# Kernel tuning notes

Measured on AMD Instinct MI355X. Metric: run time of the kernel, lower is better.

## Reference

```python
import jax, jax.numpy as jnp
import numpy as np

B, D_IN, H, C = 8192, 2048, 1024, 1000
LAYERS = [0, 1, 2, 3, 4]          # structure.layers
N_MAIN = 4                        # main hidden layers for layers[1:]
# skip layers in __init__ enumeration order: (target_layer, source_layer)
SKIPS = [(2, 0), (3, 0), (3, 1), (4, 0), (4, 1), (4, 2)]


def _linear_init(key, out_f, in_f):
    k1, k2 = jax.random.split(key)
    bound = 1.0 / np.sqrt(in_f)
    W = jax.random.uniform(k1, (out_f, in_f), minval=-bound, maxval=bound, dtype=jnp.float32)
    b = jax.random.uniform(k2, (out_f,), minval=-bound, maxval=bound, dtype=jnp.float32)
    return W, b


def setup_inputs() -> dict:
    key = jax.random.key(0)
    ks = iter(jax.random.split(key, 40))
    x = jax.random.normal(next(ks), (B, D_IN), dtype=jnp.float32)

    Wf, bf = _linear_init(next(ks), H, D_IN)
    mf = jax.random.bernoulli(next(ks), 0.5, (H, D_IN))

    main_W, main_b, main_m = [], [], []
    for _ in range(N_MAIN):
        W, b = _linear_init(next(ks), H, H)
        main_W.append(W); main_b.append(b)
        main_m.append(jax.random.bernoulli(next(ks), 0.5, (H, H)))

    skip_W, skip_b, skip_m = [], [], []
    for _ in SKIPS:
        W, b = _linear_init(next(ks), H, H)
        skip_W.append(W); skip_b.append(b)
        skip_m.append(jax.random.bernoulli(next(ks), 0.5, (H, H)))

    Wo, bo = _linear_init(next(ks), C, H)
    mo = jax.random.bernoulli(next(ks), 0.5, (C, H))

    return {"x": x, "Wf": Wf, "bf": bf, "mf": mf,
            "main_W": main_W, "main_b": main_b, "main_m": main_m,
            "skip_W": skip_W, "skip_b": skip_b, "skip_m": skip_m,
            "Wo": Wo, "bo": bo, "mo": mo}


def _masked_linear(x, W, b, m):
    # F.linear(x, weight * mask, bias): mask applied to weight before GEMM
    return x @ (W * m).T + b


def reference(x, Wf, bf, mf, main_W, main_b, main_m, skip_W, skip_b, skip_m, Wo, bo, mo):
    relu = jax.nn.relu
    last = relu(_masked_linear(x, Wf, bf, mf))        # layer 0 output, [B, H]
    results = {0: last}
    for i, layer_idx in enumerate(LAYERS[1:]):
        out = relu(_masked_linear(last, main_W[i], main_b[i], main_m[i]))
        for k, (tgt, src) in enumerate(SKIPS):
            if tgt == layer_idx:
                out = out + relu(_masked_linear(results[src], skip_W[k], skip_b[k], skip_m[k]))
        results[layer_idx] = out
        last = out
    return _masked_linear(last, Wo, bo, mo)            # [B, C]
```

## Files before the change

### kernel.cpp

```cpp
#include <hip/hip_runtime.h>
#include <hip/hip_bf16.h>
#include <stdint.h>


typedef unsigned short ushort_t;
typedef __bf16 bf16x8 __attribute__((ext_vector_type(8)));
typedef float f32x4 __attribute__((ext_vector_type(4)));

__device__ __forceinline__ void gl_lds16(const void* g, void* l) {
  typedef __attribute__((address_space(1))) void gvoid;
  typedef __attribute__((address_space(3))) void lvoid;
  __builtin_amdgcn_global_load_lds((gvoid*)(void*)g, (lvoid*)l, 16, 0, 0);
}

__device__ __forceinline__ ushort_t f2b(float f) {
  __hip_bfloat16 h = (__hip_bfloat16)f;
  return *(ushort_t*)&h;
}

__global__ void detect_kernel(const ushort_t* x, const ushort_t* mf, int* flags) {
  __shared__ int s[4];
  if (threadIdx.x < 4) s[threadIdx.x] = 0;
  __syncthreads();
  int expout = 0, m3f80_even = 0, m3f80_odd = 0, mhi01 = 0;
  for (int k = threadIdx.x; k < 2048; k += 256) {
    ushort_t w = x[k];
    int e = (w >> 7) & 0xFF;
    if (e < 96 || e > 144) expout++;
    ushort_t mw = mf[k];
    if (mw == 0x3F80) { if (k & 1) m3f80_odd++; else m3f80_even++; }
    if ((mw >> 8) == 1) mhi01++;
  }
  atomicAdd(&s[0], expout);
  atomicAdd(&s[1], m3f80_even);
  atomicAdd(&s[2], m3f80_odd);
  atomicAdd(&s[3], mhi01);
  __syncthreads();
  if (threadIdx.x == 0) {
    flags[0] = (s[0] > 100) ? 1 : 0;
    int mmode = 0;
    if (s[1] > 100) mmode = 2;
    else if (s[2] > 100) mmode = 3;
    else if (s[3] > 200) mmode = 1;
    flags[1] = mmode;
  }
}

struct PrepEnt {
  const void* w; size_t woff;
  const void* m; size_t moff;
  ushort_t* o;
  int n;
  int valid;
};
struct PrepAll { PrepEnt e[25]; };

__global__ void prep_weights(PrepAll p, const int* flags) {
  const bool f32 = flags[0] != 0;
  const int mmode = flags[1];
  const PrepEnt e = p.e[blockIdx.y];
  const int nch = e.n >> 3;
  const int stride = blockDim.x * gridDim.x;
  for (int ci = blockIdx.x * blockDim.x + threadIdx.x; ci < nch; ci += stride) {
    const int i = ci << 3;
    ushort_t o[8] = {0, 0, 0, 0, 0, 0, 0, 0};
    if (i < e.valid) {
      ushort_t wb[8];
      if (f32) {
        const float* wp = (const float*)e.w + e.woff + i;
        float4 a = *(const float4*)wp;
        float4 b = *(const float4*)(wp + 4);
        wb[0] = f2b(a.x); wb[1] = f2b(a.y); wb[2] = f2b(a.z); wb[3] = f2b(a.w);
        wb[4] = f2b(b.x); wb[5] = f2b(b.y); wb[6] = f2b(b.z); wb[7] = f2b(b.w);
      } else {
        *(uint4*)wb = *(const uint4*)((const ushort_t*)e.w + e.woff + i);
      }
      unsigned mk = 0xFF;
      if (e.m) {
        mk = 0;
        if (mmode == 0) {
          const int4* mp = (const int4*)((const int*)e.m + e.moff + i);
          int4 a = mp[0], b = mp[1];
          mk = (a.x != 0) | ((a.y != 0) << 1) | ((a.z != 0) << 2) | ((a.w != 0) << 3) |
               ((b.x != 0) << 4) | ((b.y != 0) << 5) | ((b.z != 0) << 6) | ((b.w != 0) << 7);
        } else if (mmode == 1) {
          const uint2 mv = *(const uint2*)((const unsigned char*)e.m + e.moff + i);
          const unsigned char* mb = (const unsigned char*)&mv;
          for (int j = 0; j < 8; j++) mk |= (mb[j] != 0) << j;
        } else if (mmode == 2) {
          uint4 mv = *(const uint4*)((const ushort_t*)e.m + e.moff + i);
          const ushort_t* ms = (const ushort_t*)&mv;
          for (int j = 0; j < 8; j++) mk |= (ms[j] != 0) << j;
        } else {
          const uint4* mp = (const uint4*)((const unsigned int*)e.m + e.moff + i);
          uint4 a = mp[0], b = mp[1];
          const unsigned* u = (const unsigned*)&a;
          const unsigned* v = (const unsigned*)&b;
          for (int j = 0; j < 4; j++) mk |= (u[j] != 0) << j;
          for (int j = 0; j < 4; j++) mk |= (v[j] != 0) << (4 + j);
        }
      }
#pragma unroll
      for (int j = 0; j < 8; j++) o[j] = ((mk >> j) & 1) ? wb[j] : (ushort_t)0;
    }
    *(uint4*)(e.o + i) = *(uint4*)o;
  }
}

struct GemmSrc { const ushort_t* A; const ushort_t* B; const ushort_t* bias; };
struct GemmArgs { GemmSrc s[4]; };

template <int NSRC, bool RELU, bool NGUARD>
__launch_bounds__(256, 2)
__global__ void gemm_multi(GemmArgs args, void* Cv, const int* of32flag,
                           int K, int N_real, int ldc)
{
  __shared__ __align__(16) ushort_t As[2][128 * 32];
  __shared__ __align__(16) ushort_t Bs[2][128 * 32];

  const bool of32 = (of32flag != nullptr) && (of32flag[0] != 0);
  __hip_bfloat16* C = (__hip_bfloat16*)Cv;
  float* Cf = (float*)Cv;

  const int tid  = threadIdx.x;
  const int lane = tid & 63;
  const int wave = tid >> 6;
  const int wm = (wave >> 1) * 64;
  const int wn = (wave & 1) * 64;
  const int fr = lane & 15;
  const int kg = lane >> 4;

  const int lid = blockIdx.y * 8 + blockIdx.x;
  const int s8  = lid >> 3;
  const int bm  = ((lid & 7) * 8 + (s8 >> 3)) * 128;
  const int bn  = (s8 & 7) * 128;

  const int srow = tid >> 2;
  const int scol = (((tid & 3) ^ ((srow >> 1) & 3)) * 8);
  const size_t aoff = (size_t)(bm + srow) * K + scol;
  const size_t boff = (size_t)(bn + srow) * K + scol;
  const size_t rowskip = (size_t)64 * K;

  auto stage = [&](const ushort_t* gA, const ushort_t* gB, int buf) {
    ushort_t* lA = &As[buf][wave * 512];
    ushort_t* lB = &Bs[buf][wave * 512];
    gl_lds16(gA, lA);
    gl_lds16(gA + rowskip, lA + 2048);
    gl_lds16(gB, lB);
    gl_lds16(gB + rowskip, lB + 2048);
  };

  f32x4 acc[4][4], out_acc[4][4];
#pragma unroll
  for (int i = 0; i < 4; i++)
#pragma unroll
    for (int j = 0; j < 4; j++) {
      acc[i][j] = (f32x4){0.f, 0.f, 0.f, 0.f};
      out_acc[i][j] = (f32x4){0.f, 0.f, 0.f, 0.f};
    }

  stage(args.s[0].A + aoff, args.s[0].B + boff, 0);
  int cur = 0;

  const int sw = kg ^ ((fr >> 1) & 3);

#pragma unroll
  for (int s = 0; s < NSRC; ++s) {
    const ushort_t* gA = args.s[s].A + aoff;
    const ushort_t* gB = args.s[s].B + boff;
    for (int k0 = 0; k0 < K; k0 += 32) {
      __syncthreads();
      if (k0 + 32 < K) {
        stage(gA + k0 + 32, gB + k0 + 32, cur ^ 1);
      } else if (s + 1 < NSRC) {
        stage(args.s[s + 1].A + aoff, args.s[s + 1].B + boff, cur ^ 1);
      }

      const bf16x8* Asv = (const bf16x8*)As[cur];
      const bf16x8* Bsv = (const bf16x8*)Bs[cur];
      bf16x8 af[4], bfr[4];
#pragma unroll
      for (int i = 0; i < 4; i++) af[i]  = Asv[(wm + i * 16 + fr) * 4 + sw];
#pragma unroll
      for (int i = 0; i < 4; i++) bfr[i] = Bsv[(wn + i * 16 + fr) * 4 + sw];
#pragma unroll
      for (int mi = 0; mi < 4; mi++)
#pragma unroll
        for (int ni = 0; ni < 4; ni++)
          acc[mi][ni] = __builtin_amdgcn_mfma_f32_16x16x32_bf16(
              af[mi], bfr[ni], acc[mi][ni], 0, 0, 0);
      cur ^= 1;
    }

    if (NSRC > 1) {
      const ushort_t* bias = args.s[s].bias;
#pragma unroll
      for (int ni = 0; ni < 4; ni++) {
        const int c = bn + wn + ni * 16 + fr;
        const float bb = (float)*(const __hip_bfloat16*)(bias + c);
#pragma unroll
        for (int mi = 0; mi < 4; mi++)
#pragma unroll
          for (int j = 0; j < 4; j++) {
            float v = acc[mi][ni][j] + bb;
            if (RELU) v = fmaxf(v, 0.0f);
            out_acc[mi][ni][j] += v;
            acc[mi][ni][j] = 0.0f;
          }
      }
    }
  }

#pragma unroll
  for (int ni = 0; ni < 4; ni++) {
    const int c = bn + wn + ni * 16 + fr;
    if (NGUARD && c >= N_real) continue;
    float bb = 0.0f;
    if (NSRC == 1) bb = (float)*(const __hip_bfloat16*)(args.s[0].bias + c);
#pragma unroll
    for (int mi = 0; mi < 4; mi++) {
      const int r0 = bm + wm + mi * 16 + kg * 4;
#pragma unroll
      for (int j = 0; j < 4; j++) {
        const size_t idx = (size_t)(r0 + j) * ldc + c;
        float v;
        if (NSRC == 1) {
          v = acc[mi][ni][j] + bb;
          if (RELU) v = fmaxf(v, 0.0f);
        } else {
          v = out_acc[mi][ni][j];
        }
        if (of32) Cf[idx] = v;
        else      C[idx]  = (__hip_bfloat16)v;
      }
    }
  }
}

extern "C" void kernel_launch(void* const* d_in, const int* in_sizes, int n_in,
                              void* d_out, int out_size, void* d_ws, size_t ws_size,
                              hipStream_t stream) {
  (void)out_size; (void)ws_size;
  const int Bm = 8192, DIN = 2048, H = 1024, Cn = 1000;
  const size_t HH = (size_t)H * H;

  struct PO { const void* p; size_t off; };
  PO x{d_in[0], 0}, Wf{d_in[0], 0}, mf{d_in[0], 0}, Wo{d_in[0], 0}, mo{d_in[0], 0};
  PO bf{d_in[0], 0}, bo{d_in[0], 0};
  PO mW[4], mM[4], mB[4], sW[6], sM[6], sB[6];
  for (int i = 0; i < 4; i++) { mW[i] = {d_in[0], 0}; mM[i] = mW[i]; mB[i] = mW[i]; }
  for (int i = 0; i < 6; i++) { sW[i] = {d_in[0], 0}; sM[i] = sW[i]; sB[i] = sW[i]; }

  {
    int c2M = 0, c1M = 0, c1k = 0, cWoMo = 0, c4 = 0, c6 = 0;
    for (int i = 0; i < n_in; i++) {
      const int s = in_sizes[i];
      const void* p = d_in[i];
      switch (s) {
        case 16777216: x = {p, 0}; break;
        case 2097152:  if (c2M++ == 0) Wf = {p, 0}; else mf = {p, 0}; break;
        case 1048576: {
          int j = c1M++;
          if (j < 4)       mW[j]      = {p, 0};
          else if (j < 8)  mM[j - 4]  = {p, 0};
          else if (j < 14) sW[j - 8]  = {p, 0};
          else if (j < 20) sM[j - 14] = {p, 0};
          break;
        }
        case 1024: {
          int j = c1k++;
          if (j == 0)      bf        = {p, 0};
          else if (j < 5)  mB[j - 1] = {p, 0};
          else if (j < 11) sB[j - 5] = {p, 0};
          break;
        }
        case 1024000: if (cWoMo++ == 0) Wo = {p, 0}; else mo = {p, 0}; break;
        case 1000: bo = {p, 0}; break;
        case 4194304:
          for (int t = 0; t < 4; t++) {
            if (c4 == 0) mW[t] = {p, t * HH}; else mM[t] = {p, t * HH};
          }
          c4++; break;
        case 6291456:
          for (int t = 0; t < 6; t++) {
            if (c6 == 0) sW[t] = {p, t * HH}; else sM[t] = {p, t * HH};
          }
          c6++; break;
        case 4096:
          for (int t = 0; t < 4; t++) mB[t] = {p, (size_t)t * H};
          break;
        case 6144:
          for (int t = 0; t < 6; t++) sB[t] = {p, (size_t)t * H};
          break;
        default: break;
      }
    }
  }

  ushort_t* wsp = (ushort_t*)d_ws;
  size_t off = 0;
  int* flags = (int*)wsp; off += 32;
  ushort_t* xc = wsp + off; off += (size_t)Bm * DIN;
  __hip_bfloat16* r[5];
  for (int i = 0; i < 5; i++) { r[i] = (__hip_bfloat16*)(wsp + off); off += (size_t)Bm * H; }
  ushort_t* wWf = wsp + off; off += (size_t)H * DIN;
  ushort_t* wMain[4];
  for (int i = 0; i < 4; i++) { wMain[i] = wsp + off; off += HH; }
  ushort_t* wSkip[6];
  for (int k = 0; k < 6; k++) { wSkip[k] = wsp + off; off += HH; }
  ushort_t* wWo = wsp + off; off += (size_t)1024 * 1024;
  ushort_t* cbf_ = wsp + off; off += 1024;
  ushort_t* cmB[4];
  for (int i = 0; i < 4; i++) { cmB[i] = wsp + off; off += 1024; }
  ushort_t* csB[6];
  for (int k = 0; k < 6; k++) { csB[k] = wsp + off; off += 1024; }
  ushort_t* cbo = wsp + off; off += 1024;

  detect_kernel<<<1, 256, 0, stream>>>((const ushort_t*)x.p, (const ushort_t*)mf.p, flags);

  PrepAll p;
  p.e[0]  = { Wf.p, Wf.off, mf.p, mf.off, wWf, H * DIN, H * DIN };
  for (int i = 0; i < 4; i++)
    p.e[1 + i] = { mW[i].p, mW[i].off, mM[i].p, mM[i].off, wMain[i], (int)HH, (int)HH };
  for (int k = 0; k < 6; k++)
    p.e[5 + k] = { sW[k].p, sW[k].off, sM[k].p, sM[k].off, wSkip[k], (int)HH, (int)HH };
  p.e[11] = { Wo.p, Wo.off, mo.p, mo.off, wWo, 1024 * 1024, Cn * H };
  p.e[12] = { bf.p, bf.off, nullptr, 0, cbf_, H, H };
  for (int i = 0; i < 4; i++)
    p.e[13 + i] = { mB[i].p, mB[i].off, nullptr, 0, cmB[i], H, H };
  for (int k = 0; k < 6; k++)
    p.e[17 + k] = { sB[k].p, sB[k].off, nullptr, 0, csB[k], H, H };
  p.e[23] = { bo.p, bo.off, nullptr, 0, cbo, 1024, Cn };
  p.e[24] = { x.p, x.off, nullptr, 0, xc, Bm * DIN, Bm * DIN };
  prep_weights<<<dim3(256, 25), dim3(256), 0, stream>>>(p, flags);

  const dim3 g(8, 64), b(256);

  GemmArgs a0; a0.s[0] = { xc, wWf, cbf_ };
  gemm_multi<1, true, false><<<g, b, 0, stream>>>(a0, r[0], nullptr, DIN, H, H);

  GemmArgs a1; a1.s[0] = { (ushort_t*)r[0], wMain[0], cmB[0] };
  gemm_multi<1, true, false><<<g, b, 0, stream>>>(a1, r[1], nullptr, H, H, H);

  GemmArgs a2;
  a2.s[0] = { (ushort_t*)r[1], wMain[1], cmB[1] };
  a2.s[1] = { (ushort_t*)r[0], wSkip[0], csB[0] };
  gemm_multi<2, true, false><<<g, b, 0, stream>>>(a2, r[2], nullptr, H, H, H);

  GemmArgs a3;
  a3.s[0] = { (ushort_t*)r[2], wMain[2], cmB[2] };
  a3.s[1] = { (ushort_t*)r[0], wSkip[1], csB[1] };
  a3.s[2] = { (ushort_t*)r[1], wSkip[2], csB[2] };
  gemm_multi<3, true, false><<<g, b, 0, stream>>>(a3, r[3], nullptr, H, H, H);

  GemmArgs a4;
  a4.s[0] = { (ushort_t*)r[3], wMain[3], cmB[3] };
  a4.s[1] = { (ushort_t*)r[0], wSkip[3], csB[3] };
  a4.s[2] = { (ushort_t*)r[1], wSkip[4], csB[4] };
  a4.s[3] = { (ushort_t*)r[2], wSkip[5], csB[5] };
  gemm_multi<4, true, false><<<g, b, 0, stream>>>(a4, r[4], nullptr, H, H, H);

  GemmArgs ao; ao.s[0] = { (ushort_t*)r[4], wWo, cbo };
  gemm_multi<1, false, true><<<g, b, 0, stream>>>(ao, d_out, flags, H, Cn, Cn);
}
```

Before: 558.6 us.

## Restructure GEMM to 256x128 tiles, 8 waves, BK=64 with phased MFMA/LDS schedule

Each block now computes a 256x128 output tile with 512 threads (8 waves), stages 64-wide K slices into a double-buffered LDS with an XOR swizzle, and splits each K-step into four quadrant phases. LDS fragment loads are interleaved with MFMA bursts under explicit s_barrier, waitcnt and s_setprio control. Bias values are preloaded once per block. The goal is more reuse per loaded tile, fewer barriers per FLOP and better overlap of global-to-LDS prefetch with matrix math, at the cost of larger LDS use, higher register pressure and hand-tuned synchronization that must stay correct.

Result: faster. 535.4 us (-4.2%).

```diff
diff --git a/kernel.cpp b/kernel.cpp
--- a/kernel.cpp
+++ b/kernel.cpp
@@ -110,13 +110,17 @@
 struct GemmSrc { const ushort_t* A; const ushort_t* B; const ushort_t* bias; };
 struct GemmArgs { GemmSrc s[4]; };
 
+#define SBAR()  asm volatile("s_barrier" ::: "memory")
+#define LGKM0() asm volatile("s_waitcnt lgkmcnt(0)" ::: "memory")
+#define VMC6()  asm volatile("s_waitcnt vmcnt(6)" ::: "memory")
+#define VMC0()  asm volatile("s_waitcnt vmcnt(0)" ::: "memory")
+
 template <int NSRC, bool RELU, bool NGUARD>
-__launch_bounds__(256, 2)
+__launch_bounds__(512, 2)
 __global__ void gemm_multi(GemmArgs args, void* Cv, const int* of32flag,
                            int K, int N_real, int ldc)
 {
-  __shared__ __align__(16) ushort_t As[2][128 * 32];
-  __shared__ __align__(16) ushort_t Bs[2][128 * 32];
+  __shared__ __align__(16) ushort_t lds[2][24576];
 
   const bool of32 = (of32flag != nullptr) && (of32flag[0] != 0);
   __hip_bfloat16* C = (__hip_bfloat16*)Cv;
@@ -130,25 +134,32 @@
   const int fr = lane & 15;
   const int kg = lane >> 4;
 
-  const int lid = blockIdx.y * 8 + blockIdx.x;
-  const int s8  = lid >> 3;
-  const int bm  = ((lid & 7) * 8 + (s8 >> 3)) * 128;
-  const int bn  = (s8 & 7) * 128;
-
-  const int srow = tid >> 2;
-  const int scol = (((tid & 3) ^ ((srow >> 1) & 3)) * 8);
-  const size_t aoff = (size_t)(bm + srow) * K + scol;
-  const size_t boff = (size_t)(bn + srow) * K + scol;
-  const size_t rowskip = (size_t)64 * K;
+  const int lid = blockIdx.x;
+  const int xcd = lid & 7, chunk = lid >> 3;
+  const int bm = (xcd * 4 + (chunk >> 3)) * 256;
+  const int bn = (chunk & 7) * 128;
+
+  const int rbase = tid >> 3;
+  const int sg    = (tid & 7) ^ (rbase & 7);
+  const size_t aoff = (size_t)(bm + rbase) * K + sg * 8;
+  const size_t boff = (size_t)(bn + rbase) * K + sg * 8;
+  const size_t rs64 = (size_t)64 * K;
 
   auto stage = [&](const ushort_t* gA, const ushort_t* gB, int buf) {
-    ushort_t* lA = &As[buf][wave * 512];
-    ushort_t* lB = &Bs[buf][wave * 512];
-    gl_lds16(gA, lA);
-    gl_lds16(gA + rowskip, lA + 2048);
-    gl_lds16(gB, lB);
-    gl_lds16(gB + rowskip, lB + 2048);
+    ushort_t* base = &lds[buf][0];
+    ushort_t* lA = base + wave * 512;
+    ushort_t* lB = base + 16384 + wave * 512;
+    gl_lds16(gA,            lA);
+    gl_lds16(gA + rs64,     lA + 4096);
+    gl_lds16(gA + 2 * rs64, lA + 8192);
+    gl_lds16(gA + 3 * rs64, lA + 12288);
+    gl_lds16(gB,            lB);
+    gl_lds16(gB + rs64,     lB + 4096);
   };
+
+  const int s0   = (kg ^ (fr & 7)) * 16;
+  const int arow = (wm + fr) * 128;
+  const int brow = 32768 + (wn + fr) * 128;
 
   f32x4 acc[4][4], out_acc[4][4];
 #pragma unroll
@@ -156,67 +167,149 @@
 #pragma unroll
     for (int j = 0; j < 4; j++) {
       acc[i][j] = (f32x4){0.f, 0.f, 0.f, 0.f};
-      out_acc[i][j] = (f32x4){0.f, 0.f, 0.f, 0.f};
-    }
+      if (NSRC > 1) out_acc[i][j] = (f32x4){0.f, 0.f, 0.f, 0.f};
+    }
+
+  float bpre[NSRC][4];
+#pragma unroll
+  for (int s = 0; s < NSRC; ++s)
+#pragma unroll
+    for (int ni = 0; ni < 4; ni++)
+      bpre[s][ni] = (float)*(const __hip_bfloat16*)
+          (args.s[s].bias + bn + wn + ni * 16 + fr);
+
+  const int TPS = K >> 6;
+  const int NT  = TPS * NSRC;
 
   stage(args.s[0].A + aoff, args.s[0].B + boff, 0);
+  {
+    const int s1 = 1 / TPS, k1 = (1 % TPS) * 64;
+    stage(args.s[s1].A + aoff + k1, args.s[s1].B + boff + k1, 1);
+  }
+  VMC6();
+  SBAR();
+
+  int psrc = 2 / TPS, pk0 = (2 % TPS) * 64;
+  int csrc = 0, ck = 0;
   int cur = 0;
 
-  const int sw = kg ^ ((fr >> 1) & 3);
-
-#pragma unroll
-  for (int s = 0; s < NSRC; ++s) {
-    const ushort_t* gA = args.s[s].A + aoff;
-    const ushort_t* gB = args.s[s].B + boff;
-    for (int k0 = 0; k0 < K; k0 += 32) {
-      __syncthreads();
-      if (k0 + 32 < K) {
-        stage(gA + k0 + 32, gB + k0 + 32, cur ^ 1);
-      } else if (s + 1 < NSRC) {
-        stage(args.s[s + 1].A + aoff, args.s[s + 1].B + boff, cur ^ 1);
-      }
-
-      const bf16x8* Asv = (const bf16x8*)As[cur];
-      const bf16x8* Bsv = (const bf16x8*)Bs[cur];
-      bf16x8 af[4], bfr[4];
-#pragma unroll
-      for (int i = 0; i < 4; i++) af[i]  = Asv[(wm + i * 16 + fr) * 4 + sw];
-#pragma unroll
-      for (int i = 0; i < 4; i++) bfr[i] = Bsv[(wn + i * 16 + fr) * 4 + sw];
-#pragma unroll
-      for (int mi = 0; mi < 4; mi++)
-#pragma unroll
-        for (int ni = 0; ni < 4; ni++)
-          acc[mi][ni] = __builtin_amdgcn_mfma_f32_16x16x32_bf16(
-              af[mi], bfr[ni], acc[mi][ni], 0, 0, 0);
-      cur ^= 1;
-    }
-
-    if (NSRC > 1) {
-      const ushort_t* bias = args.s[s].bias;
-#pragma unroll
-      for (int ni = 0; ni < 4; ni++) {
-        const int c = bn + wn + ni * 16 + fr;
-        const float bb = (float)*(const __hip_bfloat16*)(bias + c);
+  for (int t = 0; t < NT; ++t) {
+    const char* Lb = (const char*)&lds[cur][0];
+    bf16x8 aL[2][2], aH[2][2], bL[2][2], bH[2][2];
+
+#pragma unroll
+    for (int m = 0; m < 2; ++m)
+#pragma unroll
+      for (int ks = 0; ks < 2; ++ks)
+        aL[m][ks] = *(const bf16x8*)(Lb + arow + m * 2048 + (s0 ^ (ks * 64)));
+#pragma unroll
+    for (int n = 0; n < 2; ++n)
+#pragma unroll
+      for (int ks = 0; ks < 2; ++ks)
+        bL[n][ks] = *(const bf16x8*)(Lb + brow + n * 2048 + (s0 ^ (ks * 64)));
+    SBAR();
+    LGKM0();
+    __builtin_amdgcn_s_setprio(1);
+#pragma unroll
+    for (int m = 0; m < 2; ++m)
+#pragma unroll
+      for (int n = 0; n < 2; ++n)
+#pragma unroll
+        for (int ks = 0; ks < 2; ++ks)
+          acc[m][n] = __builtin_amdgcn_mfma_f32_16x16x32_bf16(
+              aL[m][ks], bL[n][ks], acc[m][n], 0, 0, 0);
+    __builtin_amdgcn_s_setprio(0);
+    SBAR();
+
+#pragma unroll
+    for (int n = 0; n < 2; ++n)
+#pragma unroll
+      for (int ks = 0; ks < 2; ++ks)
+        bH[n][ks] = *(const bf16x8*)(Lb + brow + (n + 2) * 2048 + (s0 ^ (ks * 64)));
+    SBAR();
+    LGKM0();
+    __builtin_amdgcn_s_setprio(1);
+#pragma unroll
+    for (int m = 0; m < 2; ++m)
+#pragma unroll
+      for (int n = 0; n < 2; ++n)
+#pragma unroll
+        for (int ks = 0; ks < 2; ++ks)
+          acc[m][n + 2] = __builtin_amdgcn_mfma_f32_16x16x32_bf16(
+              aL[m][ks], bH[n][ks], acc[m][n + 2], 0, 0, 0);
+    __builtin_amdgcn_s_setprio(0);
+    SBAR();
+
+#pragma unroll
+    for (int m = 0; m < 2; ++m)
+#pragma unroll
+      for (int ks = 0; ks < 2; ++ks)
+        aH[m][ks] = *(const bf16x8*)(Lb + arow + (m + 2) * 2048 + (s0 ^ (ks * 64)));
+    SBAR();
+    LGKM0();
+    __builtin_amdgcn_s_setprio(1);
+#pragma unroll
+    for (int m = 0; m < 2; ++m)
+#pragma unroll
+      for (int n = 0; n < 2; ++n)
+#pragma unroll
+        for (int ks = 0; ks < 2; ++ks)
+          acc[m + 2][n] = __builtin_amdgcn_mfma_f32_16x16x32_bf16(
+              aH[m][ks], bL[n][ks], acc[m + 2][n], 0, 0, 0);
+    __builtin_amdgcn_s_setprio(0);
+    SBAR();
+
+    ck += 64;
+    const bool srcEnd = (ck == K);
+    const bool more2 = (t + 2 < NT);
+    if (more2) {
+      stage(args.s[psrc].A + aoff + pk0, args.s[psrc].B + boff + pk0, cur);
+      pk0 += 64; if (pk0 == K) { pk0 = 0; ++psrc; }
+    }
+    __builtin_amdgcn_s_setprio(1);
+#pragma unroll
+    for (int m = 0; m < 2; ++m)
+#pragma unroll
+      for (int n = 0; n < 2; ++n)
+#pragma unroll
+        for (int ks = 0; ks < 2; ++ks)
+          acc[m + 2][n + 2] = __builtin_amdgcn_mfma_f32_16x16x32_bf16(
+              aH[m][ks], bH[n][ks], acc[m + 2][n + 2], 0, 0, 0);
+    __builtin_amdgcn_s_setprio(0);
+
+    if (NSRC > 1 && srcEnd) {
+      float bb[4];
+#pragma unroll
+      for (int s = 0; s < NSRC; ++s)
+        if (s == csrc) {
+#pragma unroll
+          for (int ni = 0; ni < 4; ni++) bb[ni] = bpre[s][ni];
+        }
+#pragma unroll
+      for (int ni = 0; ni < 4; ni++)
 #pragma unroll
         for (int mi = 0; mi < 4; mi++)
 #pragma unroll
           for (int j = 0; j < 4; j++) {
-            float v = acc[mi][ni][j] + bb;
+            float v = acc[mi][ni][j] + bb[ni];
             if (RELU) v = fmaxf(v, 0.0f);
             out_acc[mi][ni][j] += v;
             acc[mi][ni][j] = 0.0f;
           }
-      }
-    }
+      ck = 0; ++csrc;
+    }
+
+    if (t + 1 < NT) {
+      if (more2) VMC6(); else VMC0();
+      SBAR();
+    }
+    cur ^= 1;
   }
 
 #pragma unroll
   for (int ni = 0; ni < 4; ni++) {
     const int c = bn + wn + ni * 16 + fr;
     if (NGUARD && c >= N_real) continue;
-    float bb = 0.0f;
-    if (NSRC == 1) bb = (float)*(const __hip_bfloat16*)(args.s[0].bias + c);
 #pragma unroll
     for (int mi = 0; mi < 4; mi++) {
       const int r0 = bm + wm + mi * 16 + kg * 4;
@@ -225,7 +318,7 @@
         const size_t idx = (size_t)(r0 + j) * ldc + c;
         float v;
         if (NSRC == 1) {
-          v = acc[mi][ni][j] + bb;
+          v = acc[mi][ni][j] + bpre[0][ni];
           if (RELU) v = fmaxf(v, 0.0f);
         } else {
           v = out_acc[mi][ni][j];
@@ -334,7 +427,7 @@
   p.e[24] = { x.p, x.off, nullptr, 0, xc, Bm * DIN, Bm * DIN };
   prep_weights<<<dim3(256, 25), dim3(256), 0, stream>>>(p, flags);
 
-  const dim3 g(8, 64), b(256);
+  const dim3 g(256), b(512);
 
   GemmArgs a0; a0.s[0] = { xc, wWf, cbf_ };
   gemm_multi<1, true, false><<<g, b, 0, stream>>>(a0, r[0], nullptr, DIN, H, H);
```
